# Performance work log

Measured on AMD Instinct MI355X. Metric: run time of the kernel, lower is better.

The kernel has to match this reference:

```python
import jax, jax.numpy as jnp
import numpy as np

NUM_CODEBOOKS = 4
CODEBOOK_SIZE = 256
EMBED_DIM = 384
BATCH = 131072


def setup_inputs() -> dict:
    key = jax.random.key(0)
    kx, kc = jax.random.split(key)
    x = jax.random.normal(kx, (BATCH, EMBED_DIM), dtype=jnp.float32)
    # torch init: uniform(-1/codebook_size, 1/codebook_size)
    codebooks = jax.random.uniform(
        kc, (NUM_CODEBOOKS, CODEBOOK_SIZE, EMBED_DIM), dtype=jnp.float32,
        minval=-1.0 / CODEBOOK_SIZE, maxval=1.0 / CODEBOOK_SIZE)
    return {"x": x, "codebooks": codebooks}


def _mse(a, b):
    return jnp.mean(jnp.square(a - b))


def reference(x, codebooks):
    sg = jax.lax.stop_gradient
    residual = x
    reconstructed = jnp.zeros_like(x)
    all_codes = []
    total_loss = jnp.float32(0.0)
    for i in range(NUM_CODEBOOKS):
        cb = codebooks[i]  # [K, D]
        # pairwise squared distances: [B, K]
        d = (jnp.sum(residual * residual, axis=-1, keepdims=True)
             + jnp.sum(cb * cb, axis=-1)
             - 2.0 * residual @ cb.T)
        codes = jnp.argmin(d, axis=-1)          # [B]
        quantized = cb[codes]                   # [B, D] gather
        cb_loss = _mse(sg(quantized), residual) + _mse(quantized, sg(residual))
        quantized_st = residual + sg(quantized - residual)  # straight-through
        reconstructed = reconstructed + quantized_st
        residual = x - reconstructed
        all_codes.append(codes)
        total_loss = total_loss + cb_loss
    codes_tensor = jnp.stack(all_codes, axis=-1)  # [B, num_codebooks]
    return reconstructed, codes_tensor, total_loss
```

## Files before the change

### kernel.cpp

```cpp
#include <hip/hip_runtime.h>
#include <hip/hip_bf16.h>

#define BATCH   131072
#define DIM     384
#define KC      256
#define NCB     4
#define ROWS    64
#define THREADS 512
#define RES_LD  388
#define NKT     12
#define NW      8
#define MARGIN  2.5e-4f

typedef __attribute__((ext_vector_type(8))) short bf16x8;
typedef __attribute__((ext_vector_type(4))) float f32x4;

__device__ __forceinline__ float pw96_sq(const float* a) {
#pragma clang fp contract(off)
    float r0 = a[0]*a[0], r1 = a[1]*a[1], r2 = a[2]*a[2], r3 = a[3]*a[3];
    float r4 = a[4]*a[4], r5 = a[5]*a[5], r6 = a[6]*a[6], r7 = a[7]*a[7];
    for (int i = 8; i < 96; i += 8) {
        r0 += a[i+0]*a[i+0]; r1 += a[i+1]*a[i+1];
        r2 += a[i+2]*a[i+2]; r3 += a[i+3]*a[i+3];
        r4 += a[i+4]*a[i+4]; r5 += a[i+5]*a[i+5];
        r6 += a[i+6]*a[i+6]; r7 += a[i+7]*a[i+7];
    }
    return ((r0+r1)+(r2+r3))+((r4+r5)+(r6+r7));
}

__global__ __launch_bounds__(256) void ccb_kernel(const float* __restrict__ cb,
                                                  float* __restrict__ bpw) {
    int i = blockIdx.x * 256 + threadIdx.x;
    if (i >= NCB * KC) return;
    const float* row = cb + (size_t)i * DIM;
    {
#pragma clang fp contract(off)
        float P0 = pw96_sq(row), P1 = pw96_sq(row + 96);
        float P2 = pw96_sq(row + 192), P3 = pw96_sq(row + 288);
        bpw[i] = (P0 + P1) + (P2 + P3);
    }
}

__global__ __launch_bounds__(256) void split_kernel(const float* __restrict__ cb,
                                                    short* __restrict__ hi,
                                                    short* __restrict__ lo) {
    int idx = blockIdx.x * 256 + threadIdx.x;
    if (idx >= NCB * NKT * KC * 32) return;
    int k    = idx & 31;
    int cand = (idx >> 5) & 255;
    int kt   = (idx >> 13) % NKT;
    int s    = idx / (NKT * KC * 32);
    float v = cb[((size_t)(s * KC + cand)) * DIM + kt * 32 + k];
    __hip_bfloat16 h = __float2bfloat16(v);
    float hv = __bfloat162float(h);
    __hip_bfloat16 l = __float2bfloat16(v - hv);
    hi[idx] = *reinterpret_cast<short*>(&h);
    lo[idx] = *reinterpret_cast<short*>(&l);
}

__device__ __forceinline__ void cvt8(const float* p, bf16x8& hi, bf16x8& lo) {
    #pragma unroll
    for (int i = 0; i < 8; ++i) {
        float v = p[i];
        __hip_bfloat16 h = __float2bfloat16(v);
        float hv = __bfloat162float(h);
        __hip_bfloat16 l = __float2bfloat16(v - hv);
        hi[i] = *reinterpret_cast<short*>(&h);
        lo[i] = *reinterpret_cast<short*>(&l);
    }
}

__global__ __launch_bounds__(512) void rq_main(const float* __restrict__ x,
                                               const float* __restrict__ cb,
                                               float* __restrict__ out,
                                               const float* __restrict__ bpw,
                                               const short* __restrict__ cbh_g,
                                               const short* __restrict__ cbl_g,
                                               double* __restrict__ loss_part) {
    __shared__ float  res[ROWS][RES_LD];
    __shared__ float  rowP[ROWS][4];
    __shared__ float  rowA[ROWS];
    __shared__ float  rowbv[ROWS];
    __shared__ int    rowbk[ROWS];
    __shared__ int    rowcnt[ROWS];
    __shared__ float  lvA[ROWS][NW];
    __shared__ int    lkA[ROWS][NW];
    __shared__ int    cntA[ROWS][NW];
    __shared__ int    codes_s[ROWS][NCB];
    __shared__ double red[THREADS];

    const int t  = threadIdx.x;
    const int w  = t >> 6;
    const int l  = t & 63;
    const int lg = l >> 4;
    const int li = l & 15;
    const int row0 = blockIdx.x * ROWS;
    const float4* x4 = (const float4*)(x + (size_t)row0 * DIM);

    float4 rec[12];
    #pragma unroll
    for (int i = 0; i < 12; ++i) rec[i] = make_float4(0.f, 0.f, 0.f, 0.f);

    double lsum = 0.0;

    for (int s = 0; s < NCB; ++s) {
        const float* cbs = cb + (size_t)s * KC * DIM;

        __syncthreads();
        #pragma unroll
        for (int i = 0; i < 12; ++i) {
            int L = i * THREADS + t;
            int r = L / 96, c4 = L % 96;
            float4 xv = x4[L];
            float4 rs;
            rs.x = xv.x - rec[i].x; rs.y = xv.y - rec[i].y;
            rs.z = xv.z - rec[i].z; rs.w = xv.w - rec[i].w;
            *(float4*)&res[r][c4 * 4] = rs;
        }
        __syncthreads();

        if (t < 256) {
            int r = t >> 2, qi = t & 3;
            rowP[r][qi] = pw96_sq(&res[r][qi * 96]);
        }
        __syncthreads();
        if (t < ROWS) {
#pragma clang fp contract(off)
            rowA[t] = (rowP[t][0] + rowP[t][1]) + (rowP[t][2] + rowP[t][3]);
        }

        f32x4 acc[4][2];
        #pragma unroll
        for (int a = 0; a < 4; ++a)
            #pragma unroll
            for (int b = 0; b < 2; ++b) acc[a][b] = (f32x4){0.f, 0.f, 0.f, 0.f};

        const size_t sbase = (size_t)s * NKT * KC * 32;
        const int    coff  = (w * 32 + li) * 32 + lg * 8;

        bf16x8 bhv[2][2], blv[2][2];
        #pragma unroll
        for (int jc = 0; jc < 2; ++jc) {
            size_t off = sbase + (size_t)(coff + jc * 512);
            bhv[0][jc] = *(const bf16x8*)(cbh_g + off);
            blv[0][jc] = *(const bf16x8*)(cbl_g + off);
        }
        #pragma unroll
        for (int kt = 0; kt < NKT; ++kt) {
            const int cur = kt & 1, nxt = cur ^ 1;
            if (kt + 1 < NKT) {
                #pragma unroll
                for (int jc = 0; jc < 2; ++jc) {
                    size_t off = sbase + (size_t)(kt + 1) * (KC * 32)
                               + (size_t)(coff + jc * 512);
                    bhv[nxt][jc] = *(const bf16x8*)(cbh_g + off);
                    blv[nxt][jc] = *(const bf16x8*)(cbl_g + off);
                }
            }
            #pragma unroll
            for (int rt = 0; rt < 4; ++rt) {
                bf16x8 ah, al;
                cvt8(&res[rt * 16 + li][kt * 32 + lg * 8], ah, al);
                #pragma unroll
                for (int jc = 0; jc < 2; ++jc) {
                    acc[rt][jc] = __builtin_amdgcn_mfma_f32_16x16x32_bf16(ah, bhv[cur][jc], acc[rt][jc], 0, 0, 0);
                    acc[rt][jc] = __builtin_amdgcn_mfma_f32_16x16x32_bf16(ah, blv[cur][jc], acc[rt][jc], 0, 0, 0);
                    acc[rt][jc] = __builtin_amdgcn_mfma_f32_16x16x32_bf16(al, bhv[cur][jc], acc[rt][jc], 0, 0, 0);
                }
            }
        }

        float ccl2[2];
        #pragma unroll
        for (int jc = 0; jc < 2; ++jc) ccl2[jc] = bpw[s * KC + w * 32 + jc * 16 + li];

        float pbv[4][4]; int pbk[4][4];
        #pragma unroll
        for (int rt = 0; rt < 4; ++rt)
            #pragma unroll
            for (int q = 0; q < 4; ++q) {
                float bv = 3.4e38f; int bk = 1 << 30;
                #pragma unroll
                for (int jc = 0; jc < 2; ++jc) {
                    float sv = ccl2[jc] - 2.0f * acc[rt][jc][q];
                    int k = w * 32 + jc * 16 + li;
                    if (sv < bv || (sv == bv && k < bk)) { bv = sv; bk = k; }
                }
                pbv[rt][q] = bv; pbk[rt][q] = bk;
            }
        #pragma unroll
        for (int m = 1; m < 16; m <<= 1) {
            #pragma unroll
            for (int rt = 0; rt < 4; ++rt)
                #pragma unroll
                for (int q = 0; q < 4; ++q) {
                    float ov = __shfl_xor(pbv[rt][q], m);
                    int   ok = __shfl_xor(pbk[rt][q], m);
                    if (ov < pbv[rt][q] || (ov == pbv[rt][q] && ok < pbk[rt][q])) {
                        pbv[rt][q] = ov; pbk[rt][q] = ok;
                    }
                }
        }
        #pragma unroll
        for (int rt = 0; rt < 4; ++rt)
            #pragma unroll
            for (int q = 0; q < 4; ++q)
                if (li == rt * 4 + q) {
                    lvA[rt * 16 + lg * 4 + q][w] = pbv[rt][q];
                    lkA[rt * 16 + lg * 4 + q][w] = pbk[rt][q];
                }
        __syncthreads();

        if (t < ROWS) {
            float bv = lvA[t][0]; int bk = lkA[t][0];
            #pragma unroll
            for (int ww = 1; ww < NW; ++ww) {
                float v = lvA[t][ww]; int k = lkA[t][ww];
                if (v < bv || (v == bv && k < bk)) { bv = v; bk = k; }
            }
            rowbv[t] = bv; rowbk[t] = bk;
        }
        __syncthreads();

        int pcnt[4][4];
        #pragma unroll
        for (int rt = 0; rt < 4; ++rt)
            #pragma unroll
            for (int q = 0; q < 4; ++q) {
                int row = rt * 16 + lg * 4 + q;
                float thr = rowbv[row] + MARGIN;
                int c = 0;
                #pragma unroll
                for (int jc = 0; jc < 2; ++jc) {
                    float sv = ccl2[jc] - 2.0f * acc[rt][jc][q];
                    c += (sv <= thr) ? 1 : 0;
                }
                pcnt[rt][q] = c;
            }
        #pragma unroll
        for (int m = 1; m < 16; m <<= 1) {
            #pragma unroll
            for (int rt = 0; rt < 4; ++rt)
                #pragma unroll
                for (int q = 0; q < 4; ++q)
                    pcnt[rt][q] += __shfl_xor(pcnt[rt][q], m);
        }
        #pragma unroll
        for (int rt = 0; rt < 4; ++rt)
            #pragma unroll
            for (int q = 0; q < 4; ++q)
                if (li == rt * 4 + q) cntA[rt * 16 + lg * 4 + q][w] = pcnt[rt][q];
        __syncthreads();
        if (t < ROWS) {
            int c = 0;
            #pragma unroll
            for (int ww = 0; ww < NW; ++ww) c += cntA[t][ww];
            rowcnt[t] = c;
            if (c == 1) codes_s[t][s] = rowbk[t] & 0xFF;
        }
        __syncthreads();

        #pragma unroll
        for (int rt = 0; rt < 4; ++rt)
            #pragma unroll
            for (int q = 0; q < 4; ++q) {
                float bd = 3.4e38f; int bk = 1 << 30;
                int row = rt * 16 + lg * 4 + q;
                if (rowcnt[row] >= 2) {
                    const float thr = rowbv[row] + MARGIN;
                    const float* rrow = &res[row][0];
                    #pragma unroll
                    for (int jc = 0; jc < 2; ++jc) {
                        float sv = ccl2[jc] - 2.0f * acc[rt][jc][q];
                        if (sv <= thr) {
                            int k = w * 32 + jc * 16 + li;
                            const float* crow = cbs + (size_t)k * DIM;
                            float a32 = 0.0f;
                            for (int d = 0; d < DIM; ++d)
                                a32 = fmaf(rrow[d], crow[d], a32);
                            float T  = rowA[row] + ccl2[jc];
                            float dv = T - 2.0f * a32;
                            if (dv < bd || (dv == bd && k < bk)) { bd = dv; bk = k; }
                        }
                    }
                }
                pbv[rt][q] = bd; pbk[rt][q] = bk;
            }
        #pragma unroll
        for (int m = 1; m < 16; m <<= 1) {
            #pragma unroll
            for (int rt = 0; rt < 4; ++rt)
                #pragma unroll
                for (int q = 0; q < 4; ++q) {
                    float ov = __shfl_xor(pbv[rt][q], m);
                    int   ok = __shfl_xor(pbk[rt][q], m);
                    if (ov < pbv[rt][q] || (ov == pbv[rt][q] && ok < pbk[rt][q])) {
                        pbv[rt][q] = ov; pbk[rt][q] = ok;
                    }
                }
        }
        #pragma unroll
        for (int rt = 0; rt < 4; ++rt)
            #pragma unroll
            for (int q = 0; q < 4; ++q)
                if (li == rt * 4 + q) {
                    lvA[rt * 16 + lg * 4 + q][w] = pbv[rt][q];
                    lkA[rt * 16 + lg * 4 + q][w] = pbk[rt][q];
                }
        __syncthreads();
        if (t < ROWS && rowcnt[t] >= 2) {
            float bv = lvA[t][0]; int bk = lkA[t][0];
            #pragma unroll
            for (int ww = 1; ww < NW; ++ww) {
                float v = lvA[t][ww]; int k = lkA[t][ww];
                if (v < bv || (v == bv && k < bk)) { bv = v; bk = k; }
            }
            codes_s[t][s] = bk & 0xFF;
        }
        __syncthreads();

        #pragma unroll
        for (int i = 0; i < 12; ++i) {
            int L = i * THREADS + t;
            int r = L / 96, c4 = L % 96;
            int code = codes_s[r][s] & 0xFF;
            float4 q  = ((const float4*)(cbs + (size_t)code * DIM))[c4];
            float4 rs = *(const float4*)&res[r][c4 * 4];
            float4 df;
            df.x = q.x - rs.x; df.y = q.y - rs.y;
            df.z = q.z - rs.z; df.w = q.w - rs.w;
            float4 qst;
            qst.x = rs.x + df.x; qst.y = rs.y + df.y;
            qst.z = rs.z + df.z; qst.w = rs.w + df.w;
            rec[i].x = rec[i].x + qst.x; rec[i].y = rec[i].y + qst.y;
            rec[i].z = rec[i].z + qst.z; rec[i].w = rec[i].w + qst.w;
            lsum = fma((double)df.x, (double)df.x, lsum);
            lsum = fma((double)df.y, (double)df.y, lsum);
            lsum = fma((double)df.z, (double)df.z, lsum);
            lsum = fma((double)df.w, (double)df.w, lsum);
        }
    }

    #pragma unroll
    for (int i = 0; i < 12; ++i) {
        int L = i * THREADS + t;
        ((float4*)out)[(size_t)blockIdx.x * (ROWS * 96) + L] = rec[i];
    }

    if (t < ROWS) {
        float4 c;
        c.x = (float)(codes_s[t][0] & 0xFF);
        c.y = (float)(codes_s[t][1] & 0xFF);
        c.z = (float)(codes_s[t][2] & 0xFF);
        c.w = (float)(codes_s[t][3] & 0xFF);
        *(float4*)&out[(size_t)BATCH * DIM + (size_t)(row0 + t) * NCB] = c;
    }

    red[t] = lsum;
    __syncthreads();
    for (int st = 256; st > 0; st >>= 1) {
        if (t < st) red[t] += red[t + st];
        __syncthreads();
    }
    if (t == 0) loss_part[blockIdx.x] = red[0];
}

__global__ __launch_bounds__(256) void loss_fin(const double* __restrict__ loss_part,
                                                float* __restrict__ out) {
    __shared__ double red[256];
    int t = threadIdx.x;
    double s = 0.0;
    for (int i = t; i < BATCH / ROWS; i += 256) s += loss_part[i];
    red[t] = s;
    __syncthreads();
    for (int st = 128; st > 0; st >>= 1) {
        if (t < st) red[t] += red[t + st];
        __syncthreads();
    }
    if (t == 0) {
        double total = red[0] * (2.0 / ((double)BATCH * (double)DIM));
        out[(size_t)BATCH * DIM + (size_t)BATCH * NCB] = (float)total;
    }
}

extern "C" void kernel_launch(void* const* d_in, const int* in_sizes, int n_in,
                              void* d_out, int out_size, void* d_ws, size_t ws_size,
                              hipStream_t stream) {
    const float* x  = (const float*)d_in[0];
    const float* cb = (const float*)d_in[1];
    float* out = (float*)d_out;

    double* loss_part = (double*)d_ws;
    float*  bpw       = (float*)((char*)d_ws + 16384);
    short*  cbh_g     = (short*)((char*)d_ws + 32768);
    short*  cbl_g     = (short*)((char*)d_ws + 32768 + 786432);

    ccb_kernel<<<dim3(4), dim3(256), 0, stream>>>(cb, bpw);
    split_kernel<<<dim3((NCB * NKT * KC * 32 + 255) / 256), dim3(256), 0, stream>>>(cb, cbh_g, cbl_g);
    rq_main<<<dim3(BATCH / ROWS), dim3(THREADS), 0, stream>>>(x, cb, out, bpw,
                                                              cbh_g, cbl_g, loss_part);
    loss_fin<<<dim3(1), dim3(256), 0, stream>>>(loss_part, out);
}
```

Baseline: 1.079 ms.

## Store residual as pre-split bf16 hi/lo in LDS, compact refinement rows into buffer

The residual is now converted to bf16 hi/lo parts once when written to shared memory, so the MFMA loop loads ready bf16x8 operands instead of converting fp32 to bf16 on every k-tile and row tile. The fp32 residual array is removed. Rows that need exact fp32 refinement are compacted into a small 8-row buffer through a ballot/popcount slot assignment, and their squared norm is computed there. The residual for the final update is recomputed from x and rec in global memory. This removes repeated conversion work and reduces LDS footprint, in exchange for extra global reloads of x and a loop over refinement batches that has extra barriers.

Result: slower. 2.124 ms (+96.9%).

```diff
diff --git a/kernel.cpp b/kernel.cpp
--- a/kernel.cpp
+++ b/kernel.cpp
@@ -7,9 +7,11 @@
 #define NCB     4
 #define ROWS    64
 #define THREADS 512
-#define RES_LD  388
 #define NKT     12
 #define NW      8
+#define NBUF    8
+#define AH_LD   392
+#define BUF_LD  388
 #define MARGIN  2.5e-4f
 
 typedef __attribute__((ext_vector_type(8))) short bf16x8;
@@ -58,16 +60,22 @@
     lo[idx] = *reinterpret_cast<short*>(&l);
 }
 
-__device__ __forceinline__ void cvt8(const float* p, bf16x8& hi, bf16x8& lo) {
-    #pragma unroll
-    for (int i = 0; i < 8; ++i) {
-        float v = p[i];
-        __hip_bfloat16 h = __float2bfloat16(v);
-        float hv = __bfloat162float(h);
-        __hip_bfloat16 l = __float2bfloat16(v - hv);
-        hi[i] = *reinterpret_cast<short*>(&h);
-        lo[i] = *reinterpret_cast<short*>(&l);
-    }
+__device__ __forceinline__ void cvt4(float4 v, ushort4& h4, ushort4& l4) {
+    float a0 = v.x, a1 = v.y, a2 = v.z, a3 = v.w;
+    __hip_bfloat16 h0 = __float2bfloat16(a0), h1 = __float2bfloat16(a1);
+    __hip_bfloat16 h2 = __float2bfloat16(a2), h3 = __float2bfloat16(a3);
+    __hip_bfloat16 l0 = __float2bfloat16(a0 - __bfloat162float(h0));
+    __hip_bfloat16 l1 = __float2bfloat16(a1 - __bfloat162float(h1));
+    __hip_bfloat16 l2 = __float2bfloat16(a2 - __bfloat162float(h2));
+    __hip_bfloat16 l3 = __float2bfloat16(a3 - __bfloat162float(h3));
+    h4.x = *reinterpret_cast<unsigned short*>(&h0);
+    h4.y = *reinterpret_cast<unsigned short*>(&h1);
+    h4.z = *reinterpret_cast<unsigned short*>(&h2);
+    h4.w = *reinterpret_cast<unsigned short*>(&h3);
+    l4.x = *reinterpret_cast<unsigned short*>(&l0);
+    l4.y = *reinterpret_cast<unsigned short*>(&l1);
+    l4.z = *reinterpret_cast<unsigned short*>(&l2);
+    l4.w = *reinterpret_cast<unsigned short*>(&l3);
 }
 
 __global__ __launch_bounds__(512) void rq_main(const float* __restrict__ x,
@@ -77,16 +85,17 @@
                                                const short* __restrict__ cbh_g,
                                                const short* __restrict__ cbl_g,
                                                double* __restrict__ loss_part) {
-    __shared__ float  res[ROWS][RES_LD];
-    __shared__ float  rowP[ROWS][4];
-    __shared__ float  rowA[ROWS];
+    __shared__ short  ahi[ROWS][AH_LD];
+    __shared__ short  alo[ROWS][AH_LD];
+    __shared__ float  buf[NBUF][BUF_LD];
     __shared__ float  rowbv[ROWS];
     __shared__ int    rowbk[ROWS];
-    __shared__ int    rowcnt[ROWS];
+    __shared__ int    rowslot[ROWS];
     __shared__ float  lvA[ROWS][NW];
     __shared__ int    lkA[ROWS][NW];
     __shared__ int    cntA[ROWS][NW];
     __shared__ int    codes_s[ROWS][NCB];
+    __shared__ int    nref_s;
     __shared__ double red[THREADS];
 
     const int t  = threadIdx.x;
@@ -105,6 +114,8 @@
 
     for (int s = 0; s < NCB; ++s) {
         const float* cbs = cb + (size_t)s * KC * DIM;
+        const size_t sbase = (size_t)s * NKT * KC * 32;
+        const int    coff  = (w * 32 + li) * 32 + lg * 8;
 
         __syncthreads();
         #pragma unroll
@@ -115,28 +126,18 @@
             float4 rs;
             rs.x = xv.x - rec[i].x; rs.y = xv.y - rec[i].y;
             rs.z = xv.z - rec[i].z; rs.w = xv.w - rec[i].w;
-            *(float4*)&res[r][c4 * 4] = rs;
-        }
-        __syncthreads();
-
-        if (t < 256) {
-            int r = t >> 2, qi = t & 3;
-            rowP[r][qi] = pw96_sq(&res[r][qi * 96]);
-        }
-        __syncthreads();
-        if (t < ROWS) {
-#pragma clang fp contract(off)
-            rowA[t] = (rowP[t][0] + rowP[t][1]) + (rowP[t][2] + rowP[t][3]);
-        }
+            ushort4 h4, l4;
+            cvt4(rs, h4, l4);
+            *(ushort4*)&ahi[r][c4 * 4] = h4;
+            *(ushort4*)&alo[r][c4 * 4] = l4;
+        }
+        __syncthreads();
 
         f32x4 acc[4][2];
         #pragma unroll
         for (int a = 0; a < 4; ++a)
             #pragma unroll
             for (int b = 0; b < 2; ++b) acc[a][b] = (f32x4){0.f, 0.f, 0.f, 0.f};
-
-        const size_t sbase = (size_t)s * NKT * KC * 32;
-        const int    coff  = (w * 32 + li) * 32 + lg * 8;
 
         bf16x8 bhv[2][2], blv[2][2];
         #pragma unroll
@@ -159,8 +160,8 @@
             }
             #pragma unroll
             for (int rt = 0; rt < 4; ++rt) {
-                bf16x8 ah, al;
-                cvt8(&res[rt * 16 + li][kt * 32 + lg * 8], ah, al);
+                bf16x8 ah = *(const bf16x8*)&ahi[rt * 16 + li][kt * 32 + lg * 8];
+                bf16x8 al = *(const bf16x8*)&alo[rt * 16 + li][kt * 32 + lg * 8];
                 #pragma unroll
                 for (int jc = 0; jc < 2; ++jc) {
                     acc[rt][jc] = __builtin_amdgcn_mfma_f32_16x16x32_bf16(ah, bhv[cur][jc], acc[rt][jc], 0, 0, 0);
@@ -251,73 +252,107 @@
             for (int q = 0; q < 4; ++q)
                 if (li == rt * 4 + q) cntA[rt * 16 + lg * 4 + q][w] = pcnt[rt][q];
         __syncthreads();
+
         if (t < ROWS) {
             int c = 0;
             #pragma unroll
             for (int ww = 0; ww < NW; ++ww) c += cntA[t][ww];
-            rowcnt[t] = c;
-            if (c == 1) codes_s[t][s] = rowbk[t] & 0xFF;
-        }
-        __syncthreads();
-
-        #pragma unroll
-        for (int rt = 0; rt < 4; ++rt)
-            #pragma unroll
-            for (int q = 0; q < 4; ++q) {
-                float bd = 3.4e38f; int bk = 1 << 30;
-                int row = rt * 16 + lg * 4 + q;
-                if (rowcnt[row] >= 2) {
-                    const float thr = rowbv[row] + MARGIN;
-                    const float* rrow = &res[row][0];
-                    #pragma unroll
-                    for (int jc = 0; jc < 2; ++jc) {
-                        float sv = ccl2[jc] - 2.0f * acc[rt][jc][q];
-                        if (sv <= thr) {
-                            int k = w * 32 + jc * 16 + li;
-                            const float* crow = cbs + (size_t)k * DIM;
-                            float a32 = 0.0f;
-                            for (int d = 0; d < DIM; ++d)
-                                a32 = fmaf(rrow[d], crow[d], a32);
-                            float T  = rowA[row] + ccl2[jc];
-                            float dv = T - 2.0f * a32;
-                            if (dv < bd || (dv == bd && k < bk)) { bd = dv; bk = k; }
+            bool need = (c >= 2);
+            if (!need) codes_s[t][s] = rowbk[t] & 0xFF;
+            unsigned long long m = __ballot(need);
+            int slot = __popcll(m & ((1ull << t) - 1ull));
+            rowslot[t] = need ? slot : -1;
+            if (t == 0) nref_s = (int)__popcll(m);
+        }
+        __syncthreads();
+        const int nref = nref_s;
+
+        for (int base = 0; base < nref; base += NBUF) {
+            #pragma unroll
+            for (int i = 0; i < 12; ++i) {
+                int L = i * THREADS + t;
+                int r = L / 96, c4 = L % 96;
+                int sl = rowslot[r];
+                if (sl >= base && sl < base + NBUF) {
+                    float4 xv = x4[L];
+                    float4 rs;
+                    rs.x = xv.x - rec[i].x; rs.y = xv.y - rec[i].y;
+                    rs.z = xv.z - rec[i].z; rs.w = xv.w - rec[i].w;
+                    *(float4*)&buf[sl - base][c4 * 4] = rs;
+                }
+            }
+            __syncthreads();
+
+            #pragma unroll
+            for (int rt = 0; rt < 4; ++rt)
+                #pragma unroll
+                for (int q = 0; q < 4; ++q) {
+                    float bd = 3.4e38f; int bk = 1 << 30;
+                    int row = rt * 16 + lg * 4 + q;
+                    int sl = rowslot[row];
+                    if (sl >= base && sl < base + NBUF) {
+                        const float* rr = &buf[sl - base][0];
+                        float A;
+                        {
+#pragma clang fp contract(off)
+                            float P0 = pw96_sq(rr), P1 = pw96_sq(rr + 96);
+                            float P2 = pw96_sq(rr + 192), P3 = pw96_sq(rr + 288);
+                            A = (P0 + P1) + (P2 + P3);
+                        }
+                        const float thr = rowbv[row] + MARGIN;
+                        #pragma unroll
+                        for (int jc = 0; jc < 2; ++jc) {
+                            float sv = ccl2[jc] - 2.0f * acc[rt][jc][q];
+                            if (sv <= thr) {
+                                int k = w * 32 + jc * 16 + li;
+                                const float* crow = cbs + (size_t)k * DIM;
+                                float a32 = 0.0f;
+                                for (int d = 0; d < DIM; ++d)
+                                    a32 = fmaf(rr[d], crow[d], a32);
+                                float T  = A + ccl2[jc];
+                                float dv = T - 2.0f * a32;
+                                if (dv < bd || (dv == bd && k < bk)) { bd = dv; bk = k; }
+                            }
                         }
                     }
-                }
-                pbv[rt][q] = bd; pbk[rt][q] = bk;
-            }
-        #pragma unroll
-        for (int m = 1; m < 16; m <<= 1) {
+                    pbv[rt][q] = bd; pbk[rt][q] = bk;
+                }
+            #pragma unroll
+            for (int m = 1; m < 16; m <<= 1) {
+                #pragma unroll
+                for (int rt = 0; rt < 4; ++rt)
+                    #pragma unroll
+                    for (int q = 0; q < 4; ++q) {
+                        float ov = __shfl_xor(pbv[rt][q], m);
+                        int   ok = __shfl_xor(pbk[rt][q], m);
+                        if (ov < pbv[rt][q] || (ov == pbv[rt][q] && ok < pbk[rt][q])) {
+                            pbv[rt][q] = ov; pbk[rt][q] = ok;
+                        }
+                    }
+            }
             #pragma unroll
             for (int rt = 0; rt < 4; ++rt)
                 #pragma unroll
-                for (int q = 0; q < 4; ++q) {
-                    float ov = __shfl_xor(pbv[rt][q], m);
-                    int   ok = __shfl_xor(pbk[rt][q], m);
-                    if (ov < pbv[rt][q] || (ov == pbv[rt][q] && ok < pbk[rt][q])) {
-                        pbv[rt][q] = ov; pbk[rt][q] = ok;
+                for (int q = 0; q < 4; ++q)
+                    if (li == rt * 4 + q) {
+                        lvA[rt * 16 + lg * 4 + q][w] = pbv[rt][q];
+                        lkA[rt * 16 + lg * 4 + q][w] = pbk[rt][q];
                     }
-                }
-        }
-        #pragma unroll
-        for (int rt = 0; rt < 4; ++rt)
-            #pragma unroll
-            for (int q = 0; q < 4; ++q)
-                if (li == rt * 4 + q) {
-                    lvA[rt * 16 + lg * 4 + q][w] = pbv[rt][q];
-                    lkA[rt * 16 + lg * 4 + q][w] = pbk[rt][q];
-                }
-        __syncthreads();
-        if (t < ROWS && rowcnt[t] >= 2) {
-            float bv = lvA[t][0]; int bk = lkA[t][0];
-            #pragma unroll
-            for (int ww = 1; ww < NW; ++ww) {
-                float v = lvA[t][ww]; int k = lkA[t][ww];
-                if (v < bv || (v == bv && k < bk)) { bv = v; bk = k; }
-            }
-            codes_s[t][s] = bk & 0xFF;
-        }
-        __syncthreads();
+            __syncthreads();
+            if (t < ROWS) {
+                int sl = rowslot[t];
+                if (sl >= base && sl < base + NBUF) {
+                    float bv = lvA[t][0]; int bk = lkA[t][0];
+                    #pragma unroll
+                    for (int ww = 1; ww < NW; ++ww) {
+                        float v = lvA[t][ww]; int k = lkA[t][ww];
+                        if (v < bv || (v == bv && k < bk)) { bv = v; bk = k; }
+                    }
+                    codes_s[t][s] = bk & 0xFF;
+                }
+            }
+            __syncthreads();
+        }
 
         #pragma unroll
         for (int i = 0; i < 12; ++i) {
@@ -325,7 +360,10 @@
             int r = L / 96, c4 = L % 96;
             int code = codes_s[r][s] & 0xFF;
             float4 q  = ((const float4*)(cbs + (size_t)code * DIM))[c4];
-            float4 rs = *(const float4*)&res[r][c4 * 4];
+            float4 xv = x4[L];
+            float4 rs;
+            rs.x = xv.x - rec[i].x; rs.y = xv.y - rec[i].y;
+            rs.z = xv.z - rec[i].z; rs.w = xv.w - rec[i].w;
             float4 df;
             df.x = q.x - rs.x; df.y = q.y - rs.y;
             df.z = q.z - rs.z; df.w = q.w - rs.w;
```
